# Kernel tuning notes

Measured on AMD Instinct MI355X. Metric: run time of the kernel, lower is better.

The kernel has to match this reference:

```python
import jax, jax.numpy as jnp
import numpy as np
import math

FACTOR = 1

def setup_inputs() -> dict:
    key = jax.random.key(0)
    kq, kk, kv = jax.random.split(key, 3)
    B, H, L, E = 8, 8, 1024, 512
    queries = jax.random.normal(kq, (B, H, L, E), dtype=jnp.float32)
    keys = jax.random.normal(kk, (B, H, L, E), dtype=jnp.float32)
    values = jax.random.normal(kv, (B, H, L, E), dtype=jnp.float32)
    return {"queries": queries, "keys": keys, "values": values}

def _time_delay_agg_full(values, corr):
    # values: [B,H,C,Len], corr: [B,H,C,Len]  (C = seq positions, Len = feature dim here)
    length = values.shape[-1]
    top_k = int(FACTOR * math.log(length))
    weights, delay = jax.lax.top_k(corr, top_k)          # [B,H,C,k]
    tmp_corr = jax.nn.softmax(weights, axis=-1)          # [B,H,C,k]
    # gather from values.repeat(...,2) at init_index + delay  ==  circular gather mod length
    idx = (jnp.arange(length)[None, None, None, None, :] + delay[..., None]) % length  # [B,H,C,k,Len]
    gathered = jnp.take_along_axis(values[:, :, :, None, :], idx, axis=-1)             # [B,H,C,k,Len]
    return jnp.einsum('bhckl,bhck->bhcl', gathered, tmp_corr)

def reference(queries, keys, values):
    B, H, L, E = queries.shape
    S = values.shape[2]
    # L == S in this setup, so pad/slice branches are no-ops; keep slice for fidelity
    values = values[:, :, :L, :]
    keys = keys[:, :, :L, :]
    q_fft = jnp.fft.fft(queries, axis=-1)
    k_fft = jnp.fft.fft(keys, axis=-1)
    res = q_fft * jnp.conj(k_fft)
    # torch.fft.irfft(res, n=E) trims the complex input to E//2+1 before inverse; numpy/jax do the same
    corr = jnp.fft.irfft(res, n=E, axis=-1).astype(queries.dtype)  # [B,H,L,E]
    V = _time_delay_agg_full(values, corr)
    return V, jnp.transpose(corr, (0, 3, 1, 2))
```

## Files before the change

### kernel.cpp

```cpp
#include <hip/hip_runtime.h>
#include <math.h>


#define TOPK 6
#define LGKM0 asm volatile("s_waitcnt lgkmcnt(0)" ::: "memory")

__device__ __forceinline__ float2 cmul(float2 a, float2 b) {
  return make_float2(fmaf(a.x, b.x, -(a.y * b.y)), fmaf(a.x, b.y, a.y * b.x));
}
__device__ __forceinline__ float2 cadd(float2 a, float2 b) { return make_float2(a.x + b.x, a.y + b.y); }
__device__ __forceinline__ float2 csub(float2 a, float2 b) { return make_float2(a.x - b.x, a.y - b.y); }
__device__ __forceinline__ float2 mnegi(float2 v) { return make_float2(v.y, -v.x); }

__device__ __forceinline__ unsigned bf16rne(float x) {
  unsigned t = __float_as_uint(x);
  return (t + 0x7FFFu + ((t >> 16) & 1u)) >> 16;
}

__device__ __forceinline__ unsigned wave_umax64(unsigned x) {
#define DPPMAX(ctrl)                                                          \
  {                                                                           \
    unsigned t = (unsigned)__builtin_amdgcn_update_dpp(0, (int)x, ctrl, 0xf,  \
                                                       0xf, true);            \
    x = t > x ? t : x;                                                        \
  }
  DPPMAX(0x111)
  DPPMAX(0x112)
  DPPMAX(0x114)
  DPPMAX(0x118)
  DPPMAX(0x142)
  DPPMAX(0x143)
#undef DPPMAX
  return (unsigned)__builtin_amdgcn_readlane((int)x, 63);
}

__device__ __forceinline__ void radix8(float2 y[8]) {
  float2 p0 = cadd(y[0], y[4]), p1 = csub(y[0], y[4]);
  float2 p2 = cadd(y[2], y[6]), p3 = csub(y[2], y[6]);
  float2 q0 = cadd(y[1], y[5]), q1 = csub(y[1], y[5]);
  float2 q2 = cadd(y[3], y[7]), q3 = csub(y[3], y[7]);
  float2 mp3 = mnegi(p3), mq3 = mnegi(q3);
  float2 E0 = cadd(p0, p2), E2 = csub(p0, p2);
  float2 E1 = cadd(p1, mp3), E3 = csub(p1, mp3);
  float2 O0 = cadd(q0, q2), O2 = csub(q0, q2);
  float2 O1 = cadd(q1, mq3), O3 = csub(q1, mq3);
  const float RT = 0.70710678118654752440f;
  float2 T1 = make_float2(RT * (O1.x + O1.y), RT * (O1.y - O1.x));
  float2 T2 = mnegi(O2);
  float2 T3 = make_float2(RT * (O3.y - O3.x), -RT * (O3.x + O3.y));
  y[0] = cadd(E0, O0); y[4] = csub(E0, O0);
  y[1] = cadd(E1, T1); y[5] = csub(E1, T1);
  y[2] = cadd(E2, T2); y[6] = csub(E2, T2);
  y[3] = cadd(E3, T3); y[7] = csub(E3, T3);
}

__device__ __forceinline__ void twiddle8(float2 y[8], float2 w) {
  float2 wp = w;
  y[1] = cmul(y[1], wp);
  wp = cmul(wp, w); y[2] = cmul(y[2], wp);
  wp = cmul(wp, w); y[3] = cmul(y[3], wp);
  wp = cmul(wp, w); y[4] = cmul(y[4], wp);
  wp = cmul(wp, w); y[5] = cmul(y[5], wp);
  wp = cmul(wp, w); y[6] = cmul(y[6], wp);
  wp = cmul(wp, w); y[7] = cmul(y[7], wp);
}

__device__ __forceinline__ void fft512t(float2 y[8], float* zx, float* zy,
                                        int u, float2 w512u, float2 w64n0) {
  const int f0 = u >> 3, n0 = u & 7;
  radix8(y);
  twiddle8(y, w512u);
#pragma unroll
  for (int r = 0; r < 8; ++r) { int s = 72 * r + u; zx[s] = y[r].x; zy[s] = y[r].y; }
  LGKM0;
#pragma unroll
  for (int j = 0; j < 8; ++j) {
    int s = 72 * f0 + 8 * j + n0;
    y[j] = make_float2(zx[s], zy[s]);
  }
  radix8(y);
  twiddle8(y, w64n0);
  LGKM0;
#pragma unroll
  for (int g = 0; g < 8; ++g) {
    int s = 72 * f0 + 8 * g + (n0 ^ g);
    zx[s] = y[g].x; zy[s] = y[g].y;
  }
  LGKM0;
#pragma unroll
  for (int j = 0; j < 8; ++j) {
    int s = 72 * f0 + 8 * n0 + (j ^ n0);
    y[j] = make_float2(zx[s], zy[s]);
  }
  radix8(y);
}

__global__ __launch_bounds__(512, 4) void autoagg_kernel(
    const float* __restrict__ q, const float* __restrict__ kk,
    const float* __restrict__ v, float* __restrict__ outV,
    float* __restrict__ outC) {
  __shared__ float zscr[8 * 1152];
  __shared__ unsigned short tile[512 * 36];
  const int tid = threadIdx.x;
  const int u = tid & 63;
  const int w = tid >> 6;
  const int bid = blockIdx.x;
  float* zx = zscr + w * 1152;
  float* zy = zx + 576;

  const int f0 = u >> 3, n0 = u & 7;
  const int base = f0 + (n0 << 3);

  const float N2PI = -6.28318530717958647692f;
  float s_, c_;
  __sincosf(N2PI * (float)u * (1.f / 512.f), &s_, &c_);
  const float2 w512u = make_float2(c_, s_);
  __sincosf(N2PI * (float)n0 * (1.f / 64.f), &s_, &c_);
  const float2 w64n0 = make_float2(c_, s_);

#pragma unroll 1
  for (int p = 0; p < 4; ++p) {
    const int row = (bid << 5) + (p << 3) + w;
    const int rowU = __builtin_amdgcn_readfirstlane(row);
    const float* qrow = q + (size_t)rowU * 512;
    const float* krow = kk + (size_t)rowU * 512;
    const float* vrow = v + (size_t)rowU * 512;

    float2 y[8];
#pragma unroll
    for (int m = 0; m < 8; ++m)
      y[m] = make_float2(qrow[u + (m << 6)], krow[u + (m << 6)]);

    fft512t(y, zx, zy, u, w512u, w64n0);

    LGKM0;
#pragma unroll
    for (int r = 0; r < 8; ++r) {
      int s = 72 * r + (n0 << 3) + f0;
      zx[s] = y[r].x; zy[s] = y[r].y;
    }
    LGKM0;
    const float SCL = 1.f / 2048.f;
#pragma unroll
    for (int m = 0; m < 8; ++m) {
      int fA = (m << 6) | u;
      int fB = (512 - fA) & 511;
      int sA = 72 * m + (f0 << 3) + n0;
      int sB = 72 * (fB >> 6) + (((fB >> 3) & 7) << 3) + (fB & 7);
      float Ax = zx[sA], Ay = zy[sA];
      float Bx = zx[sB], By = zy[sB];
      float sx = Ax + Bx, sy = Ay - By;
      float dx = Ax - Bx, dy = Ay + By;
      y[m] = make_float2((sx * dy - sy * dx) * SCL,
                         -fmaf(sx, dx, sy * dy) * SCL);
    }

    fft512t(y, zx, zy, u, w512u, w64n0);

    const int col = (p << 3) | w;
#pragma unroll
    for (int r = 0; r < 8; ++r)
      tile[(base + (r << 6)) * 36 + col] = (unsigned short)bf16rne(y[r].x);

    unsigned key[8];
#pragma unroll
    for (int r = 0; r < 8; ++r) {
      unsigned bb = __float_as_uint(y[r].x);
      unsigned sgn = (unsigned)((int)bb >> 31);
      unsigned mono = bb ^ (sgn | 0x80000000u);
      key[r] = (mono & 0xFFFFFE00u) | (unsigned)(511 - (base + (r << 6)));
    }
    float w0 = 0.f, tw[TOPK]; int dly[TOPK];
#pragma unroll
    for (int it = 0; it < TOPK; ++it) {
      unsigned km = key[0];
#pragma unroll
      for (int i = 1; i < 8; ++i) km = key[i] > km ? key[i] : km;
      unsigned kmax = wave_umax64(km);
      unsigned mb = kmax & 0xFFFFFE00u;
      unsigned vb = (mb & 0x80000000u) ? (mb ^ 0x80000000u) : ~mb;
      float val = __uint_as_float(vb);
      if (it == 0) w0 = val;
      tw[it] = __expf(val - w0);
      dly[it] = 511 - (int)(kmax & 0x1FFu);
#pragma unroll
      for (int i = 0; i < 8; ++i) if (key[i] == kmax) key[i] = 0u;
    }
    float ssum = 0.f;
#pragma unroll
    for (int it = 0; it < TOPK; ++it) ssum += tw[it];
    const float inv = 1.f / ssum;

    float V[8] = {0.f, 0.f, 0.f, 0.f, 0.f, 0.f, 0.f, 0.f};
#pragma unroll
    for (int it = 0; it < TOPK; ++it) {
      const float twk = tw[it] * inv;
      const int d = dly[it];
#pragma unroll
      for (int i = 0; i < 8; ++i)
        V[i] = fmaf(twk, vrow[(base + (i << 6) + d) & 511], V[i]);
    }

    LGKM0;
#pragma unroll
    for (int i = 0; i < 8; ++i)
      zx[76 * i + 9 * n0 + f0] = V[i];
    LGKM0;
    float vt[8];
#pragma unroll
    for (int j = 0; j < 8; ++j)
      vt[j] = zx[76 * f0 + 9 * n0 + j];
    LGKM0;
    float4* ov = (float4*)(outV + (size_t)rowU * 512 + (u << 3));
    ov[0] = make_float4(vt[0], vt[1], vt[2], vt[3]);
    ov[1] = make_float4(vt[4], vt[5], vt[6], vt[7]);
  }

  __syncthreads();
  const int b9 = bid >> 8;
  const int h9 = (bid >> 5) & 7;
  const int l0 = (bid & 31) << 5;
#pragma unroll
  for (int round = 0; round < 8; ++round) {
    int e = (round << 6) + (tid >> 3);
    int lq = (tid & 7) << 2;
    const unsigned short* tr = tile + e * 36 + lq;
    float4 tv = make_float4(__uint_as_float((unsigned)tr[0] << 16),
                            __uint_as_float((unsigned)tr[1] << 16),
                            __uint_as_float((unsigned)tr[2] << 16),
                            __uint_as_float((unsigned)tr[3] << 16));
    *(float4*)(outC + (((size_t)b9 * 512 + e) * 8 + h9) * 1024 + l0 + lq) = tv;
  }
}

extern "C" void kernel_launch(void* const* d_in, const int* in_sizes, int n_in,
                              void* d_out, int out_size, void* d_ws, size_t ws_size,
                              hipStream_t stream) {
  const float* q = (const float*)d_in[0];
  const float* k = (const float*)d_in[1];
  const float* v = (const float*)d_in[2];
  float* outV = (float*)d_out;
  float* outC = (float*)d_out + (size_t)8 * 8 * 1024 * 512;
  dim3 grid(65536 / 32), block(512);
  hipLaunchKernelGGL(autoagg_kernel, grid, block, 0, stream, q, k, v, outV, outC);
}
```

Measured before the change: 230.6 us.

## Pair conjugate FFT bins via wave shuffles and remap second FFT to natural order

```diff
diff --git a/kernel.cpp b/kernel.cpp
--- a/kernel.cpp
+++ b/kernel.cpp
@@ -66,12 +66,12 @@
 }
 
 __device__ __forceinline__ void fft512t(float2 y[8], float* zx, float* zy,
-                                        int u, float2 w512u, float2 w64n0) {
-  const int f0 = u >> 3, n0 = u & 7;
+                                        int role, float2 w512, float2 w64) {
+  const int f0 = role >> 3, n0 = role & 7;
   radix8(y);
-  twiddle8(y, w512u);
-#pragma unroll
-  for (int r = 0; r < 8; ++r) { int s = 72 * r + u; zx[s] = y[r].x; zy[s] = y[r].y; }
+  twiddle8(y, w512);
+#pragma unroll
+  for (int r = 0; r < 8; ++r) { int s = 72 * r + role; zx[s] = y[r].x; zy[s] = y[r].y; }
   LGKM0;
 #pragma unroll
   for (int j = 0; j < 8; ++j) {
@@ -79,7 +79,7 @@
     y[j] = make_float2(zx[s], zy[s]);
   }
   radix8(y);
-  twiddle8(y, w64n0);
+  twiddle8(y, w64);
   LGKM0;
 #pragma unroll
   for (int g = 0; g < 8; ++g) {
@@ -110,6 +110,7 @@
 
   const int f0 = u >> 3, n0 = u & 7;
   const int base = f0 + (n0 << 3);
+  const int up = (u >= 8) ? (71 - u) : (u ? (8 - u) : 0);
 
   const float N2PI = -6.28318530717958647692f;
   float s_, c_;
@@ -117,6 +118,10 @@
   const float2 w512u = make_float2(c_, s_);
   __sincosf(N2PI * (float)n0 * (1.f / 64.f), &s_, &c_);
   const float2 w64n0 = make_float2(c_, s_);
+  __sincosf(N2PI * (float)base * (1.f / 512.f), &s_, &c_);
+  const float2 w512b = make_float2(c_, s_);
+  __sincosf(N2PI * (float)f0 * (1.f / 64.f), &s_, &c_);
+  const float2 w64f0 = make_float2(c_, s_);
 
 #pragma unroll 1
   for (int p = 0; p < 4; ++p) {
@@ -133,34 +138,31 @@
 
     fft512t(y, zx, zy, u, w512u, w64n0);
 
-    LGKM0;
+    float2 pB[8];
 #pragma unroll
     for (int r = 0; r < 8; ++r) {
-      int s = 72 * r + (n0 << 3) + f0;
-      zx[s] = y[r].x; zy[s] = y[r].y;
-    }
-    LGKM0;
+      pB[r].x = __shfl(y[7 - r].x, up, 64);
+      pB[r].y = __shfl(y[7 - r].y, up, 64);
+    }
+    if (u == 0) {
+#pragma unroll
+      for (int r = 0; r < 8; ++r) pB[r] = y[(8 - r) & 7];
+    }
     const float SCL = 1.f / 2048.f;
 #pragma unroll
-    for (int m = 0; m < 8; ++m) {
-      int fA = (m << 6) | u;
-      int fB = (512 - fA) & 511;
-      int sA = 72 * m + (f0 << 3) + n0;
-      int sB = 72 * (fB >> 6) + (((fB >> 3) & 7) << 3) + (fB & 7);
-      float Ax = zx[sA], Ay = zy[sA];
-      float Bx = zx[sB], By = zy[sB];
-      float sx = Ax + Bx, sy = Ay - By;
-      float dx = Ax - Bx, dy = Ay + By;
-      y[m] = make_float2((sx * dy - sy * dx) * SCL,
+    for (int r = 0; r < 8; ++r) {
+      float sx = y[r].x + pB[r].x, sy = y[r].y - pB[r].y;
+      float dx = y[r].x - pB[r].x, dy = y[r].y + pB[r].y;
+      y[r] = make_float2((sx * dy - sy * dx) * SCL,
                          -fmaf(sx, dx, sy * dy) * SCL);
     }
 
-    fft512t(y, zx, zy, u, w512u, w64n0);
+    fft512t(y, zx, zy, base, w512b, w64f0);
 
     const int col = (p << 3) | w;
 #pragma unroll
     for (int r = 0; r < 8; ++r)
-      tile[(base + (r << 6)) * 36 + col] = (unsigned short)bf16rne(y[r].x);
+      tile[(u + (r << 6)) * 36 + col] = (unsigned short)bf16rne(y[r].x);
 
     unsigned key[8];
 #pragma unroll
@@ -168,7 +170,7 @@
       unsigned bb = __float_as_uint(y[r].x);
       unsigned sgn = (unsigned)((int)bb >> 31);
       unsigned mono = bb ^ (sgn | 0x80000000u);
-      key[r] = (mono & 0xFFFFFE00u) | (unsigned)(511 - (base + (r << 6)));
+      key[r] = (mono & 0xFFFFFE00u) | (unsigned)(511 - (u + (r << 6)));
     }
     float w0 = 0.f, tw[TOPK]; int dly[TOPK];
 #pragma unroll
@@ -198,22 +200,12 @@
       const int d = dly[it];
 #pragma unroll
       for (int i = 0; i < 8; ++i)
-        V[i] = fmaf(twk, vrow[(base + (i << 6) + d) & 511], V[i]);
-    }
-
-    LGKM0;
-#pragma unroll
-    for (int i = 0; i < 8; ++i)
-      zx[76 * i + 9 * n0 + f0] = V[i];
-    LGKM0;
-    float vt[8];
-#pragma unroll
-    for (int j = 0; j < 8; ++j)
-      vt[j] = zx[76 * f0 + 9 * n0 + j];
-    LGKM0;
-    float4* ov = (float4*)(outV + (size_t)rowU * 512 + (u << 3));
-    ov[0] = make_float4(vt[0], vt[1], vt[2], vt[3]);
-    ov[1] = make_float4(vt[4], vt[5], vt[6], vt[7]);
+        V[i] = fmaf(twk, vrow[(u + (i << 6) + d) & 511], V[i]);
+    }
+
+    float* ovr = outV + (size_t)rowU * 512;
+#pragma unroll
+    for (int i = 0; i < 8; ++i) ovr[u + (i << 6)] = V[i];
   }
 
   __syncthreads();
```

Measured after the change: 309.1 us. +34.0%, slower.
